# Kernel tuning notes

Measured on AMD Instinct MI355X. Metric: run time of the kernel, lower is better.

The kernel has to match this reference:

```python
import jax, jax.numpy as jnp
import numpy as np
from functools import partial

B, S, A = 128, 256, 8
V, E, H, C, HOPS = 50000, 300, 300, 3, 3

def _lstm_dir(x, lens, Wih, Whh, bih, bhh):
    # x: [B,S,E]; masked (packed-style) LSTM: padded steps don't update state, output 0
    b, s, _ = x.shape
    h_dim = Whh.shape[1]
    xg = jnp.einsum('bse,ge->bsg', x, Wih) + bih  # [B,S,4H]
    mask = (jnp.arange(s)[None, :] < lens[:, None])  # [B,S]

    def step(carry, inp):
        h, c = carry
        xg_t, m = inp  # [B,4H], [B]
        g = xg_t + h @ Whh.T + bhh
        i, f, gg, o = jnp.split(g, 4, axis=-1)
        i = jax.nn.sigmoid(i); f = jax.nn.sigmoid(f)
        gg = jnp.tanh(gg); o = jax.nn.sigmoid(o)
        c_new = f * c + i * gg
        h_new = o * jnp.tanh(c_new)
        m2 = m[:, None]
        h2 = jnp.where(m2, h_new, h)
        c2 = jnp.where(m2, c_new, c)
        out = jnp.where(m2, h_new, 0.0)
        return (h2, c2), out

    z = jnp.zeros((b, h_dim), x.dtype)
    _, outs = jax.lax.scan(step, (z, z), (xg.transpose(1, 0, 2), mask.T))
    return outs.transpose(1, 0, 2)

def _bilstm(x, lens, Wih_f, Whh_f, bih_f, bhh_f, Wih_b, Whh_b, bih_b, bhh_b):
    out_f = _lstm_dir(x, lens, Wih_f, Whh_f, bih_f, bhh_f)
    s = x.shape[1]
    t = jnp.arange(s)[None, :]
    # reverse each sequence within its own valid length
    idx = jnp.where(t < lens[:, None], lens[:, None] - 1 - t, t)  # [B,S]
    x_rev = jnp.take_along_axis(x, idx[:, :, None], axis=1)
    out_b_rev = _lstm_dir(x_rev, lens, Wih_b, Whh_b, bih_b, bhh_b)
    out_b = jnp.take_along_axis(out_b_rev, idx[:, :, None], axis=1)
    return jnp.concatenate([out_f, out_b], axis=-1)  # [B,S,2H]

def _locationed_memory(memory, mem_len, left_len, asp_len):
    b, s, _ = memory.shape
    pos = jnp.arange(s, dtype=memory.dtype)[None, :]  # [1,S]
    ml = mem_len[:, None].astype(memory.dtype)
    ll = left_len[:, None].astype(memory.dtype)
    al = asp_len[:, None].astype(memory.dtype)
    in_left = pos < ll
    in_right = (pos >= ll + al) & (pos < ml)
    w = jnp.where(in_left, 1.0 - (ll - pos) / ml,
        jnp.where(in_right, 1.0 - (pos - ll - al + 1.0) / ml, 1.0))
    u = jnp.where(in_left, pos - ll,
        jnp.where(in_right, pos - ll - al + 1.0, 0.0))
    v = memory * w[:, :, None]
    return jnp.concatenate([v, u[:, :, None]], axis=2)  # [B,S,2H+1]

def _gru_cell(x, h, Wih, Whh, bih, bhh):
    gi = x @ Wih.T + bih
    gh = h @ Whh.T + bhh
    i_r, i_z, i_n = jnp.split(gi, 3, axis=-1)
    h_r, h_z, h_n = jnp.split(gh, 3, axis=-1)
    r = jax.nn.sigmoid(i_r + h_r)
    z = jax.nn.sigmoid(i_z + h_z)
    n = jnp.tanh(i_n + r * h_n)
    return (1.0 - z) * n + z * h

def setup_inputs() -> dict:
    key = jax.random.key(0)
    ks = jax.random.split(key, 24)
    mem_len = jax.random.randint(ks[0], (B,), S // 2, S + 1)
    asp_len = jax.random.randint(ks[1], (B,), 1, A + 1)
    max_left = mem_len - asp_len
    left_len = jax.random.randint(ks[2], (B,), 0, 10**6) % (max_left + 1)

    def make_ids(k, n, lens):
        tok = jax.random.randint(k, (B, n), 1, V)
        return jnp.where(jnp.arange(n)[None, :] < lens[:, None], tok, 0)

    text = make_ids(ks[3], S, mem_len)
    aspect = make_ids(ks[4], A, asp_len)
    left_context = make_ids(ks[5], S, left_len)

    def nrm(k, shape, scale=0.05):
        return jax.random.normal(k, shape, jnp.float32) * scale

    params = dict(
        embedding=nrm(ks[6], (V, E), 0.1),
        Wih_f=nrm(ks[7], (4 * H, E)), Whh_f=nrm(ks[8], (4 * H, H)),
        bih_f=nrm(ks[9], (4 * H,)), bhh_f=nrm(ks[10], (4 * H,)),
        Wih_b=nrm(ks[11], (4 * H, E)), Whh_b=nrm(ks[12], (4 * H, H)),
        bih_b=nrm(ks[13], (4 * H,)), bhh_b=nrm(ks[14], (4 * H,)),
        att_W=nrm(ks[15], (1, 2 * H + 1 + 2 * E)), att_b=nrm(ks[16], (1,)),
        gru_Wih=nrm(ks[17], (3 * E, 2 * H + 1)), gru_Whh=nrm(ks[18], (3 * E, E)),
        gru_bih=nrm(ks[19], (3 * E,)), gru_bhh=nrm(ks[20], (3 * E,)),
        dense_W=nrm(ks[21], (C, E)), dense_b=nrm(ks[22], (C,)),
    )
    return dict(text=text, aspect=aspect, left_context=left_context, **params)

def reference(text, aspect, left_context, embedding,
              Wih_f, Whh_f, bih_f, bhh_f, Wih_b, Whh_b, bih_b, bhh_b,
              att_W, att_b, gru_Wih, gru_Whh, gru_bih, gru_bhh,
              dense_W, dense_b):
    left_len = jnp.sum(left_context != 0, axis=-1)
    mem_len = jnp.sum(text != 0, axis=-1)
    asp_len = jnp.sum(aspect != 0, axis=-1)

    memory = embedding[text]  # [B,S,E]
    memory = _bilstm(memory, mem_len, Wih_f, Whh_f, bih_f, bhh_f,
                     Wih_b, Whh_b, bih_b, bhh_b)  # [B,S,2H]
    memory = _locationed_memory(memory, mem_len, left_len, asp_len)  # [B,S,2H+1]

    asp_emb = jnp.sum(embedding[aspect], axis=1) / asp_len[:, None].astype(jnp.float32)  # [B,E]

    et = jnp.zeros_like(asp_emb)
    b, s, _ = memory.shape
    for _ in range(HOPS):
        a = jnp.concatenate([
            memory,
            jnp.broadcast_to(et[:, None, :], (b, s, et.shape[-1])),
            jnp.broadcast_to(asp_emb[:, None, :], (b, s, asp_emb.shape[-1])),
        ], axis=-1)  # [B,S,2H+1+2E]
        g = jnp.einsum('bsd,od->bso', a, att_W) + att_b  # [B,S,1]
        alpha = jax.nn.softmax(g, axis=1)
        i = jnp.einsum('bso,bsd->bd', alpha, memory)  # [B,2H+1]
        et = _gru_cell(i, et, gru_Wih, gru_Whh, gru_bih, gru_bhh)
    return et @ dense_W.T + dense_b  # [B,C]
```

## Files before the change

### kernel.cpp

```cpp
#include <hip/hip_runtime.h>
#include <hip/hip_bf16.h>
#include <math.h>

#define B_ 128
#define S_ 256
#define A_ 8
#define E_ 300
#define H_ 300
#define KPAD 320
#define NGU 16
#define NGB 4
#define NCOL 80
#define WROW 648
#define HROW 328
#define NBLK 128

typedef unsigned short u16;
typedef unsigned int u32;
typedef unsigned long long u64;
typedef __attribute__((ext_vector_type(8))) short short8;
typedef __attribute__((ext_vector_type(4))) float floatx4;
typedef __attribute__((ext_vector_type(4))) unsigned int u32x4;

#define MFMA16(a, b, c) __builtin_amdgcn_mfma_f32_16x16x32_bf16((a), (b), (c), 0, 0, 0)

__device__ __host__ __forceinline__ int gu_cnt(int g) { return g < 6 ? 20 : 18; }
__device__ __host__ __forceinline__ int gu_u0(int g) { return g < 6 ? 20 * g : 120 + 18 * (g - 6); }

static constexpr size_t oLens = 0;
static constexpr size_t oFlg  = 1536;
static constexpr size_t oH    = 4096;
static constexpr size_t oMemX = 331776;
static constexpr size_t oWp   = 42274816;
static constexpr size_t oBp   = 45551616;
static constexpr size_t oMemV = 45561856;
static constexpr size_t oIT   = 124205056;
static constexpr size_t oGi   = 124512768;
static constexpr size_t oGh   = 124973568;
static constexpr size_t oEt   = 125434368;
static constexpr size_t oSc   = 125587968;
static constexpr size_t WS_NEED = 125719040;

__device__ __forceinline__ u16 f2bf(float f) {
  union { float f; unsigned u; } v; v.f = f;
  unsigned r = (v.u + 0x7FFFu + ((v.u >> 16) & 1u)) >> 16;
  return (u16)r;
}
__device__ __forceinline__ float sigm(float x) { return 1.f / (1.f + __expf(-x)); }
__device__ __forceinline__ float tanh_f(float x) {
  x = fminf(15.f, fmaxf(-15.f, x));
  float e = __expf(2.f * x);
  return (e - 1.f) / (e + 1.f);
}

__global__ __launch_bounds__(256) void init_kernel(const int* __restrict__ text,
                                                   const int* __restrict__ aspect,
                                                   const int* __restrict__ leftc,
                                                   char* __restrict__ ws) {
  const int bid = blockIdx.x, tid = threadIdx.x;
  if (bid == 0) {
    if (tid < B_) {
      int c = 0; const int* p = text + tid * S_;
      for (int s = 0; s < S_; ++s) c += (p[s] != 0);
      ((int*)(ws + oLens))[tid] = c;
    }
  } else if (bid == 1) {
    if (tid < B_) {
      int c = 0; const int* p = leftc + tid * S_;
      for (int s = 0; s < S_; ++s) c += (p[s] != 0);
      ((int*)(ws + oLens + 512))[tid] = c;
    }
  } else if (bid == 2) {
    if (tid < B_) {
      int c = 0; const int* p = aspect + tid * A_;
      for (int s = 0; s < A_; ++s) c += (p[s] != 0);
      ((int*)(ws + oLens + 1024))[tid] = c;
    }
  } else {
    const int CW = 640, HW = 327680 / 4, EW = 153600 / 4;
    const int total = CW + HW + EW;
    for (int i = (bid - 3) * 256 + tid; i < total; i += 64 * 256) {
      if (i < CW)            ((unsigned*)(ws + oFlg))[i] = 0u;
      else if (i < CW + HW)  ((unsigned*)(ws + oH))[i - CW] = 0u;
      else                   ((unsigned*)(ws + oEt))[i - CW - HW] = 0u;
    }
  }
}

__global__ __launch_bounds__(256) void pack_kernel(
    const float* __restrict__ WihF, const float* __restrict__ WhhF,
    const float* __restrict__ bihF, const float* __restrict__ bhhF,
    const float* __restrict__ WihB, const float* __restrict__ WhhB,
    const float* __restrict__ bihB, const float* __restrict__ bhhB,
    char* __restrict__ ws) {
  const int WTOT = 2 * NGU * NCOL * 640;
  int idx = blockIdx.x * 256 + threadIdx.x;
  if (idx < WTOT) {
    int k = idx % 640;
    int n = (idx / 640) % NCOL;
    int g = (idx / (640 * NCOL)) % NGU;
    int dir = idx / (640 * NCOL * NGU);
    float v = 0.f;
    const int cnt = gu_cnt(g), u0 = gu_u0(g);
    if (n < cnt * 4) {
      int col = (n & 3) * 300 + u0 + (n >> 2);
      const float* Wih = dir ? WihB : WihF;
      const float* Whh = dir ? WhhB : WhhF;
      if (k < 300)                  v = Wih[(size_t)col * 300 + k];
      else if (k >= 320 && k < 620) v = Whh[(size_t)col * 300 + (k - 320)];
    }
    ((u16*)(ws + oWp))[idx] = f2bf(v);
  } else {
    int j = idx - WTOT;
    if (j < 2 * NGU * NCOL) {
      int n = j % NCOL; int g = (j / NCOL) % NGU; int dir = j / (NCOL * NGU);
      float v = 0.f;
      const int cnt = gu_cnt(g), u0 = gu_u0(g);
      if (n < cnt * 4) {
        int col = (n & 3) * 300 + u0 + (n >> 2);
        v = (dir ? bihB : bihF)[col] + (dir ? bhhB : bhhF)[col];
      }
      ((float*)(ws + oBp))[j] = v;
    }
  }
}

__global__ __launch_bounds__(KPAD) void gather_kernel(const int* __restrict__ text,
                                                      const float* __restrict__ emb,
                                                      char* __restrict__ ws) {
  const int bid = blockIdx.x;
  const int t = bid & 255;
  const int b = (bid >> 8) & 127;
  const int dir = bid >> 15;
  const int len = ((const int*)(ws + oLens))[b];
  const int tp = (dir == 0) ? t : ((t < len) ? (len - 1 - t) : t);
  const int tok = text[b * S_ + tp];
  u16* dst = (u16*)(ws + oMemX) + ((size_t)((dir * B_ + b) * S_ + t)) * KPAD;
  const float* src = emb + (size_t)tok * E_;
  const int k = threadIdx.x;
  float v = (k < E_) ? src[k] : 0.f;
  dst[k] = f2bf(v);
}

__global__ __launch_bounds__(256, 1) void lstm_kernel(char* __restrict__ ws) {
  const int bid = (int)blockIdx.x;
  const int dir = bid >> 6;
  const int gb  = (bid >> 4) & 3;
  const int g   = bid & 15;
  const int cnt = gu_cnt(g), u0 = gu_u0(g);
  const int npair = cnt >> 1;
  const int tid = threadIdx.x;
  const int wv = tid >> 6;
  const int lane = tid & 63;
  const int quad = lane >> 4;
  const int l16 = lane & 15;
  const int Mtile = wv >> 1;
  const int nt0 = (wv & 1) ? 3 : 0;
  const int ntc = (wv & 1) ? 2 : 3;

  const u64* __restrict__ Wp64 = (const u64*)(ws + oWp) + (size_t)(dir * NGU + g) * NCOL * 160;
  const float* __restrict__ Bpk = (const float*)(ws + oBp) + (dir * NGU + g) * NCOL;
  const u16* __restrict__ memx = (const u16*)(ws + oMemX) + (size_t)dir * B_ * S_ * KPAD;
  const u16* __restrict__ hb16 = (const u16*)(ws + oH);
  u32* __restrict__ hb32 = (u32*)(ws + oH);
  float* __restrict__ memv = (float*)(ws + oMemV);
  u32* __restrict__ flags = (u32*)(ws + oFlg) + (size_t)(dir * 4 + gb) * 64;

  __shared__ __align__(16) u16 Wlds[NCOL * WROW];
  __shared__ __align__(16) u16 hLds[32 * HROW];
  __shared__ float gatesLds[32 * 81];
  __shared__ float cS[640];
  __shared__ float hS[640];
  __shared__ float biasS[NCOL];
  __shared__ int lenS[32], llS[32], alS[32];

  for (int i = tid; i < NCOL * 160; i += 256) {
    int n = i / 160, k4 = i - n * 160;
    ((u64*)Wlds)[n * 162 + k4] = Wp64[i];
  }
  for (int i = tid; i < 640; i += 256) { cS[i] = 0.f; hS[i] = 0.f; }
  if (tid < NCOL) biasS[tid] = Bpk[tid];
  if (tid < 32) {
    lenS[tid] = ((const int*)(ws + oLens))[gb * 32 + tid];
    llS[tid]  = ((const int*)(ws + oLens + 512))[gb * 32 + tid];
    alS[tid]  = ((const int*)(ws + oLens + 1024))[gb * 32 + tid];
  }
  __syncthreads();

  const int row = gb * 32 + Mtile * 16 + l16;
  const u16* wq = Wlds + l16 * WROW + quad * 8;

  int eoff[5]; u16* ldst[5];
  #pragma unroll
  for (int it = 0; it < 5; ++it) {
    int e = (it * 256 + tid) * 8;
    int r = e / KPAD, c = e - r * KPAD;
    eoff[it] = e;
    ldst[it] = hLds + r * HROW + c;
  }
  const u16* hA = hLds + (Mtile * 16 + l16) * HROW + quad * 8;

  short8 xv[10];
  {
    const u16* xr = memx + ((size_t)row * S_) * KPAD + quad * 8;
    #pragma unroll
    for (int kk = 0; kk < 10; ++kk) xv[kk] = *(const short8*)(xr + kk * 32);
  }

  for (int t = 0; t < S_; ++t) {
    if (t > 0) {
      if (wv == 0) {
        const u32 target = (u32)t;
        u32 f;
        bool first = true;
        do {
          if (!first) __builtin_amdgcn_s_sleep(1);
          first = false;
          f = 0xFFFFFFFFu;
          if (lane < NGU)
            f = __hip_atomic_load(&flags[lane * 4], __ATOMIC_RELAXED, __HIP_MEMORY_SCOPE_AGENT);
        } while (!__all((int)(f >= target)));
      }
      __syncthreads();
      __builtin_amdgcn_fence(__ATOMIC_ACQUIRE, "workgroup");
    }

    u32x4 hstash[5];
    {
      const u16* hpan = hb16 + (((size_t)(t & 1) * 2 + dir) * B_ + gb * 32) * KPAD;
      #pragma unroll
      for (int it = 0; it < 5; ++it) {
        asm volatile("global_load_dwordx4 %0, %1, off sc1"
                     : "=v"(hstash[it]) : "v"(hpan + eoff[it]) : "memory");
      }
    }

    floatx4 acc[3];
    acc[0] = (floatx4){0.f, 0.f, 0.f, 0.f}; acc[1] = acc[0]; acc[2] = acc[0];
    #pragma unroll
    for (int kk = 0; kk < 10; ++kk) {
      const int ko = kk * 32;
      #pragma unroll
      for (int j = 0; j < 3; ++j) {
        if (j < ntc)
          acc[j] = MFMA16(xv[kk], *(const short8*)(wq + (nt0 + j) * 16 * WROW + ko), acc[j]);
      }
    }

    asm volatile("s_waitcnt vmcnt(0)" ::: "memory");
    #pragma unroll
    for (int it = 0; it < 5; ++it) *(u32x4*)ldst[it] = hstash[it];
    __syncthreads();

    #pragma unroll
    for (int kk = 0; kk < 10; ++kk) {
      const short8 av = *(const short8*)(hA + kk * 32);
      const int ko = 320 + kk * 32;
      #pragma unroll
      for (int j = 0; j < 3; ++j) {
        if (j < ntc)
          acc[j] = MFMA16(av, *(const short8*)(wq + (nt0 + j) * 16 * WROW + ko), acc[j]);
      }
    }

    #pragma unroll
    for (int j = 0; j < 3; ++j) {
      if (j < ntc) {
        const int colb = (nt0 + j) * 16 + l16;
        const int rb = Mtile * 16 + quad * 4;
        #pragma unroll
        for (int r = 0; r < 4; ++r)
          gatesLds[(rb + r) * 81 + colb] = acc[j][r];
      }
    }
    __syncthreads();

    const int nxt = (t + 1) & 1;
    float2 sv[2]; float* sa[2]; bool sval[2];
    #pragma unroll
    for (int z = 0; z < 2; ++z) {
      const int it = tid + z * 256;
      sval[z] = (it < 32 * npair);
      if (!sval[z]) continue;
      const int bl = it & 31;
      const int pl = it >> 5;
      const int ul0 = pl * 2;
      const int len = lenS[bl];
      const bool m = (t < len);
      const float* gp = gatesLds + bl * 81 + ul0 * 4;
      const float* bp = biasS + ul0 * 4;
      float h0K, h1K, h0N, h1N;
      {
        float ig = sigm(gp[0] + bp[0]);
        float fg = sigm(gp[1] + bp[1]);
        float gt = tanh_f(gp[2] + bp[2]);
        float og = sigm(gp[3] + bp[3]);
        float cOld = cS[ul0 * 32 + bl], hOld = hS[ul0 * 32 + bl];
        float cNew = fg * cOld + ig * gt;
        float hNew = og * tanh_f(cNew);
        cS[ul0 * 32 + bl] = m ? cNew : cOld;
        h0K = m ? hNew : hOld;
        hS[ul0 * 32 + bl] = h0K;
        h0N = m ? hNew : 0.f;
      }
      {
        float ig = sigm(gp[4] + bp[4]);
        float fg = sigm(gp[5] + bp[5]);
        float gt = tanh_f(gp[6] + bp[6]);
        float og = sigm(gp[7] + bp[7]);
        float cOld = cS[(ul0 + 1) * 32 + bl], hOld = hS[(ul0 + 1) * 32 + bl];
        float cNew = fg * cOld + ig * gt;
        float hNew = og * tanh_f(cNew);
        cS[(ul0 + 1) * 32 + bl] = m ? cNew : cOld;
        h1K = m ? hNew : hOld;
        hS[(ul0 + 1) * 32 + bl] = h1K;
        h1N = m ? hNew : 0.f;
      }
      const int bglob = gb * 32 + bl;
      u32 packed = (u32)f2bf(h0K) | ((u32)f2bf(h1K) << 16);
      __hip_atomic_store(&hb32[(((size_t)nxt * 2 + dir) * B_ + bglob) * 160 + ((u0 + ul0) >> 1)],
                         packed, __ATOMIC_RELAXED, __HIP_MEMORY_SCOPE_AGENT);
      int pos = (dir == 0) ? t : (m ? (len - 1 - t) : t);
      float ml = (float)len, ll = (float)llS[bl], al = (float)alS[bl];
      float p = (float)pos;
      float wl;
      if (p < ll) wl = 1.f - (ll - p) / ml;
      else if ((p >= ll + al) && (p < ml)) wl = 1.f - (p - ll - al + 1.f) / ml;
      else wl = 1.f;
      sv[z] = make_float2(h0N * wl, h1N * wl);
      sa[z] = &memv[((size_t)bglob * S_ + pos) * 600 + dir * 300 + u0 + ul0];
    }

    __builtin_amdgcn_fence(__ATOMIC_RELEASE, "workgroup");
    __syncthreads();
    if (tid == 0)
      __hip_atomic_store(&flags[g * 4], (u32)(t + 1), __ATOMIC_RELAXED, __HIP_MEMORY_SCOPE_AGENT);

    #pragma unroll
    for (int z = 0; z < 2; ++z)
      if (sval[z]) *(float2*)sa[z] = sv[z];
    if (t + 1 < S_) {
      const u16* xr = memx + ((size_t)row * S_ + (t + 1)) * KPAD + quad * 8;
      #pragma unroll
      for (int kk = 0; kk < 10; ++kk) xv[kk] = *(const short8*)(xr + kk * 32);
    }
  }
}

__global__ __launch_bounds__(256) void score_kernel(const float* __restrict__ attW,
                                                    char* __restrict__ ws) {
  const int bid = blockIdx.x;
  const int b = bid >> 1, sh = bid & 1;
  const int tid = threadIdx.x, wv = tid >> 6, lane = tid & 63;
  __shared__ float aW[601];
  for (int i = tid; i < 601; i += 256) aW[i] = attW[i];
  const float* memv = (const float*)(ws + oMemV) + (size_t)b * S_ * 600;
  const float ml = (float)((const int*)(ws + oLens))[b];
  const float ll = (float)((const int*)(ws + oLens + 512))[b];
  const float al = (float)((const int*)(ws + oLens + 1024))[b];
  __syncthreads();
  float* scg = (float*)(ws + oSc) + b * S_;
  for (int s = sh * 128 + wv; s < sh * 128 + 128; s += 4) {
    const float* rowp = memv + (size_t)s * 600;
    float acc = 0.f;
    for (int d = lane; d < 600; d += 64) acc += rowp[d] * aW[d];
    for (int off = 32; off; off >>= 1) acc += __shfl_xor(acc, off);
    if (lane == 0) {
      float p = (float)s;
      bool inl = p < ll;
      bool inr = (p >= ll + al) && (p < ml);
      float u = inl ? (p - ll) : (inr ? (p - ll - al + 1.f) : 0.f);
      scg[s] = acc + u * aW[600];
    }
  }
}

__global__ __launch_bounds__(256) void attn_kernel(char* __restrict__ ws) {
  const int bid = blockIdx.x;
  const int b = bid >> 1, dh = bid & 1;
  const int tid = threadIdx.x, wv = tid >> 6, lane = tid & 63;
  __shared__ float alpha[256];
  __shared__ float red[8];
  const float* scg = (const float*)(ws + oSc) + b * S_;
  float v = scg[tid];
  float mx = v;
  for (int off = 32; off; off >>= 1) mx = fmaxf(mx, __shfl_xor(mx, off));
  if (lane == 0) red[wv] = mx;
  __syncthreads();
  mx = fmaxf(fmaxf(red[0], red[1]), fmaxf(red[2], red[3]));
  float e = __expf(v - mx);
  float sm = e;
  for (int off = 32; off; off >>= 1) sm += __shfl_xor(sm, off);
  if (lane == 0) red[4 + wv] = sm;
  __syncthreads();
  float tot = red[4] + red[5] + red[6] + red[7];
  alpha[tid] = e / tot;
  const float ml = (float)((const int*)(ws + oLens))[b];
  const float ll = (float)((const int*)(ws + oLens + 512))[b];
  const float al = (float)((const int*)(ws + oLens + 1024))[b];
  __syncthreads();
  const float* memv = (const float*)(ws + oMemV) + (size_t)b * S_ * 600;
  float* iT = (float*)(ws + oIT);
  const int d0 = dh * 301, d1 = dh ? 601 : 301;
  for (int d = d0 + tid; d < d1; d += 256) {
    float acc = 0.f;
    if (d < 600) {
      for (int s = 0; s < 256; ++s) acc += alpha[s] * memv[(size_t)s * 600 + d];
    } else {
      for (int s = 0; s < 256; ++s) {
        float p = (float)s;
        bool inl = p < ll;
        bool inr = (p >= ll + al) && (p < ml);
        float u = inl ? (p - ll) : (inr ? (p - ll - al + 1.f) : 0.f);
        acc += alpha[s] * u;
      }
    }
    iT[d * 128 + b] = acc;
  }
}

__global__ __launch_bounds__(256) void gi_kernel(const float* __restrict__ Wih,
                                                 const float* __restrict__ bih,
                                                 char* __restrict__ ws) {
  int idx = blockIdx.x * 256 + threadIdx.x;
  int r = idx >> 7, b = idx & 127;
  if (r >= 900) return;
  const float* iT = (const float*)(ws + oIT);
  const float* wr = Wih + (size_t)r * 601;
  float acc = bih[r];
  for (int d = 0; d < 601; ++d) acc += iT[d * 128 + b] * wr[d];
  ((float*)(ws + oGi))[r * 128 + b] = acc;
}

__global__ __launch_bounds__(256) void gh_kernel(const float* __restrict__ Whh,
                                                 const float* __restrict__ bhh,
                                                 char* __restrict__ ws) {
  int idx = blockIdx.x * 256 + threadIdx.x;
  int r = idx >> 7, b = idx & 127;
  if (r >= 900) return;
  const float* et = (const float*)(ws + oEt);
  const float* wr = Whh + (size_t)r * 300;
  float acc = bhh[r];
  for (int u = 0; u < 300; ++u) acc += et[u * 128 + b] * wr[u];
  ((float*)(ws + oGh))[r * 128 + b] = acc;
}

__global__ __launch_bounds__(256) void up_kernel(char* __restrict__ ws) {
  int idx = blockIdx.x * 256 + threadIdx.x;
  int u = idx >> 7, b = idx & 127;
  if (u >= 300) return;
  const float* gi = (const float*)(ws + oGi);
  const float* gh = (const float*)(ws + oGh);
  float* et = (float*)(ws + oEt);
  float rr = sigm(gi[u * 128 + b] + gh[u * 128 + b]);
  float zz = sigm(gi[(300 + u) * 128 + b] + gh[(300 + u) * 128 + b]);
  float nn = tanh_f(gi[(600 + u) * 128 + b] + rr * gh[(600 + u) * 128 + b]);
  float old = et[u * 128 + b];
  et[u * 128 + b] = (1.f - zz) * nn + zz * old;
}

__global__ __launch_bounds__(384) void dense_kernel(const float* __restrict__ dW,
                                                    const float* __restrict__ dB,
                                                    float* __restrict__ out,
                                                    const char* __restrict__ ws) {
  int tid = threadIdx.x;
  if (tid >= 384) return;
  int b = tid / 3, c = tid - 3 * (tid / 3);
  const float* et = (const float*)(ws + oEt);
  float acc = dB[c];
  const float* wr = dW + c * 300;
  for (int u = 0; u < 300; ++u) acc += et[u * 128 + b] * wr[u];
  out[b * 3 + c] = acc;
}

extern "C" void kernel_launch(void* const* d_in, const int* in_sizes, int n_in,
                              void* d_out, int out_size, void* d_ws, size_t ws_size,
                              hipStream_t stream) {
  const int* text = (const int*)d_in[0];
  const int* aspect = (const int*)d_in[1];
  const int* leftc = (const int*)d_in[2];
  const float* emb = (const float*)d_in[3];
  const float* WihF = (const float*)d_in[4];
  const float* WhhF = (const float*)d_in[5];
  const float* bihF = (const float*)d_in[6];
  const float* bhhF = (const float*)d_in[7];
  const float* WihB = (const float*)d_in[8];
  const float* WhhB = (const float*)d_in[9];
  const float* bihB = (const float*)d_in[10];
  const float* bhhB = (const float*)d_in[11];
  const float* attW = (const float*)d_in[12];
  const float* gruWih = (const float*)d_in[14];
  const float* gruWhh = (const float*)d_in[15];
  const float* gruBih = (const float*)d_in[16];
  const float* gruBhh = (const float*)d_in[17];
  const float* denseW = (const float*)d_in[18];
  const float* denseB = (const float*)d_in[19];
  float* out = (float*)d_out;
  char* ws = (char*)d_ws;
  if (ws_size < WS_NEED) return;

  init_kernel<<<67, 256, 0, stream>>>(text, aspect, leftc, ws);
  pack_kernel<<<6420, 256, 0, stream>>>(WihF, WhhF, bihF, bhhF, WihB, WhhB, bihB, bhhB, ws);
  gather_kernel<<<2 * B_ * S_, KPAD, 0, stream>>>(text, emb, ws);
  lstm_kernel<<<NBLK, 256, 0, stream>>>(ws);
  score_kernel<<<2 * B_, 256, 0, stream>>>(attW, ws);
  attn_kernel<<<2 * B_, 256, 0, stream>>>(ws);
  gi_kernel<<<450, 256, 0, stream>>>(gruWih, gruBih, ws);
  for (int h = 0; h < 3; ++h) {
    gh_kernel<<<450, 256, 0, stream>>>(gruWhh, gruBhh, ws);
    up_kernel<<<150, 256, 0, stream>>>(ws);
  }
  dense_kernel<<<1, 384, 0, stream>>>(denseW, denseB, out, ws);
}
```

Measured before the change: 1.958 ms.

## Co-locate LSTM pod blocks and sync through L2-scoped flags with device-scope fallback

Remaps block IDs so the 16 blocks of each direction/batch pod are interleaved (bid&7 = pod), aiming to place them on the same XCD. Adds a second flag array and hidden-state buffer that are read with sc0 (L2-local) loads rather than device-coherent loads. If the local flags appear to lag the mirrored device-scope flags, the block switches to the device-coherent path. This targets per-timestep cross-block synchronisation latency, but it depends on an assumed block-to-XCD mapping and uses volatile/non-atomic writes, which risks stale reads or extra spinning.

Result: faster. 1.911 ms (-2.4%).

```diff
diff --git a/kernel.cpp b/kernel.cpp
--- a/kernel.cpp
+++ b/kernel.cpp
@@ -9,7 +9,6 @@
 #define H_ 300
 #define KPAD 320
 #define NGU 16
-#define NGB 4
 #define NCOL 80
 #define WROW 648
 #define HROW 328
@@ -39,7 +38,9 @@
 static constexpr size_t oGh   = 124973568;
 static constexpr size_t oEt   = 125434368;
 static constexpr size_t oSc   = 125587968;
-static constexpr size_t WS_NEED = 125719040;
+static constexpr size_t oMirr = 125719040;
+static constexpr size_t oHL2  = 125721088;
+static constexpr size_t WS_NEED = 126048768;
 
 __device__ __forceinline__ u16 f2bf(float f) {
   union { float f; unsigned u; } v; v.f = f;
@@ -51,6 +52,12 @@
   x = fminf(15.f, fmaxf(-15.f, x));
   float e = __expf(2.f * x);
   return (e - 1.f) / (e + 1.f);
+}
+__device__ __forceinline__ u32 ld_sc0(const u32* p) {
+  u32 v;
+  asm volatile("global_load_dword %0, %1, off sc0\n\ts_waitcnt vmcnt(0)"
+               : "=v"(v) : "v"(p) : "memory");
+  return v;
 }
 
 __global__ __launch_bounds__(256) void init_kernel(const int* __restrict__ text,
@@ -77,12 +84,15 @@
       ((int*)(ws + oLens + 1024))[tid] = c;
     }
   } else {
-    const int CW = 640, HW = 327680 / 4, EW = 153600 / 4;
-    const int total = CW + HW + EW;
+    const int F1 = 512, F2 = 512, HW = 81920, H2 = 81920, EW = 38400;
+    const int total = F1 + F2 + HW + H2 + EW;
     for (int i = (bid - 3) * 256 + tid; i < total; i += 64 * 256) {
-      if (i < CW)            ((unsigned*)(ws + oFlg))[i] = 0u;
-      else if (i < CW + HW)  ((unsigned*)(ws + oH))[i - CW] = 0u;
-      else                   ((unsigned*)(ws + oEt))[i - CW - HW] = 0u;
+      int j = i;
+      if (j < F1)            { ((u32*)(ws + oFlg))[j] = 0u; continue; }  j -= F1;
+      if (j < F2)            { ((u32*)(ws + oMirr))[j] = 0u; continue; } j -= F2;
+      if (j < HW)            { ((u32*)(ws + oH))[j] = 0u; continue; }    j -= HW;
+      if (j < H2)            { ((u32*)(ws + oHL2))[j] = 0u; continue; }  j -= H2;
+      ((u32*)(ws + oEt))[j] = 0u;
     }
   }
 }
@@ -144,9 +154,10 @@
 
 __global__ __launch_bounds__(256, 1) void lstm_kernel(char* __restrict__ ws) {
   const int bid = (int)blockIdx.x;
-  const int dir = bid >> 6;
-  const int gb  = (bid >> 4) & 3;
-  const int g   = bid & 15;
+  const int pod = bid & 7;
+  const int dir = pod >> 2;
+  const int gb  = pod & 3;
+  const int g   = bid >> 3;
   const int cnt = gu_cnt(g), u0 = gu_u0(g);
   const int npair = cnt >> 1;
   const int tid = threadIdx.x;
@@ -163,8 +174,11 @@
   const u16* __restrict__ memx = (const u16*)(ws + oMemX) + (size_t)dir * B_ * S_ * KPAD;
   const u16* __restrict__ hb16 = (const u16*)(ws + oH);
   u32* __restrict__ hb32 = (u32*)(ws + oH);
+  const u16* __restrict__ hl16 = (const u16*)(ws + oHL2);
+  u32* __restrict__ hl32 = (u32*)(ws + oHL2);
   float* __restrict__ memv = (float*)(ws + oMemV);
-  u32* __restrict__ flags = (u32*)(ws + oFlg) + (size_t)(dir * 4 + gb) * 64;
+  u32* __restrict__ flagsP = (u32*)(ws + oFlg) + (size_t)pod * 64;
+  u32* __restrict__ flagsM = (u32*)(ws + oMirr) + (size_t)pod * 64;
 
   __shared__ __align__(16) u16 Wlds[NCOL * WROW];
   __shared__ __align__(16) u16 hLds[32 * HROW];
@@ -173,6 +187,7 @@
   __shared__ float hS[640];
   __shared__ float biasS[NCOL];
   __shared__ int lenS[32], llS[32], alS[32];
+  __shared__ int remoteS;
 
   for (int i = tid; i < NCOL * 160; i += 256) {
     int n = i / 160, k4 = i - n * 160;
@@ -185,6 +200,7 @@
     llS[tid]  = ((const int*)(ws + oLens + 512))[gb * 32 + tid];
     alS[tid]  = ((const int*)(ws + oLens + 1024))[gb * 32 + tid];
   }
+  if (tid == 0) remoteS = 0;
   __syncthreads();
 
   const int row = gb * 32 + Mtile * 16 + l16;
@@ -211,27 +227,46 @@
     if (t > 0) {
       if (wv == 0) {
         const u32 target = (u32)t;
-        u32 f;
-        bool first = true;
-        do {
-          if (!first) __builtin_amdgcn_s_sleep(1);
-          first = false;
-          f = 0xFFFFFFFFu;
+        int spin = 0;
+        while (true) {
+          u32 f = 0xFFFFFFFFu;
+          const int rm = *(volatile int*)&remoteS;
           if (lane < NGU)
-            f = __hip_atomic_load(&flags[lane * 4], __ATOMIC_RELAXED, __HIP_MEMORY_SCOPE_AGENT);
-        } while (!__all((int)(f >= target)));
+            f = rm ? __hip_atomic_load(&flagsM[lane * 4], __ATOMIC_RELAXED, __HIP_MEMORY_SCOPE_AGENT)
+                   : ld_sc0(&flagsP[lane * 4]);
+          if (__all((int)(f >= target))) break;
+          ++spin;
+          if (!rm && spin > 64 && (spin & 15) == 0) {
+            u32 fm = 0u, fp = 0xFFFFFFFFu;
+            if (lane < NGU) {
+              fm = __hip_atomic_load(&flagsM[lane * 4], __ATOMIC_RELAXED, __HIP_MEMORY_SCOPE_AGENT);
+              fp = ld_sc0(&flagsP[lane * 4]);
+            }
+            if (__any((int)(fm > fp))) { if (lane == 0) *(volatile int*)&remoteS = 1; }
+          }
+          if (rm) __builtin_amdgcn_s_sleep(1);
+        }
       }
       __syncthreads();
       __builtin_amdgcn_fence(__ATOMIC_ACQUIRE, "workgroup");
     }
 
+    const int rem = *(volatile int*)&remoteS;
     u32x4 hstash[5];
     {
-      const u16* hpan = hb16 + (((size_t)(t & 1) * 2 + dir) * B_ + gb * 32) * KPAD;
-      #pragma unroll
-      for (int it = 0; it < 5; ++it) {
-        asm volatile("global_load_dwordx4 %0, %1, off sc1"
-                     : "=v"(hstash[it]) : "v"(hpan + eoff[it]) : "memory");
+      const size_t pbase = (((size_t)(t & 1) * 2 + dir) * B_ + gb * 32) * KPAD;
+      if (rem) {
+        const u16* hpan = hb16 + pbase;
+        #pragma unroll
+        for (int it = 0; it < 5; ++it)
+          asm volatile("global_load_dwordx4 %0, %1, off sc1"
+                       : "=v"(hstash[it]) : "v"(hpan + eoff[it]) : "memory");
+      } else {
+        const u16* hpan = hl16 + pbase;
+        #pragma unroll
+        for (int it = 0; it < 5; ++it)
+          asm volatile("global_load_dwordx4 %0, %1, off sc0"
+                       : "=v"(hstash[it]) : "v"(hpan + eoff[it]) : "memory");
       }
     }
 
@@ -317,9 +352,11 @@
         h1N = m ? hNew : 0.f;
       }
       const int bglob = gb * 32 + bl;
+      const size_t hidx = (((size_t)nxt * 2 + dir) * B_ + bglob) * 160 + ((u0 + ul0) >> 1);
       u32 packed = (u32)f2bf(h0K) | ((u32)f2bf(h1K) << 16);
-      __hip_atomic_store(&hb32[(((size_t)nxt * 2 + dir) * B_ + bglob) * 160 + ((u0 + ul0) >> 1)],
-                         packed, __ATOMIC_RELAXED, __HIP_MEMORY_SCOPE_AGENT);
+      hl32[hidx] = packed;
+      __hip_atomic_store(&hb32[hidx], packed,
+                         __ATOMIC_RELAXED, __HIP_MEMORY_SCOPE_AGENT);
       int pos = (dir == 0) ? t : (m ? (len - 1 - t) : t);
       float ml = (float)len, ll = (float)llS[bl], al = (float)alS[bl];
       float p = (float)pos;
@@ -333,8 +370,11 @@
 
     __builtin_amdgcn_fence(__ATOMIC_RELEASE, "workgroup");
     __syncthreads();
-    if (tid == 0)
-      __hip_atomic_store(&flags[g * 4], (u32)(t + 1), __ATOMIC_RELAXED, __HIP_MEMORY_SCOPE_AGENT);
+    if (tid == 0) {
+      *(volatile u32*)&flagsP[g * 4] = (u32)(t + 1);
+      __hip_atomic_store(&flagsM[g * 4], (u32)(t + 1),
+                         __ATOMIC_RELAXED, __HIP_MEMORY_SCOPE_AGENT);
+    }
 
     #pragma unroll
     for (int z = 0; z < 2; ++z)
```
